# Kernel optimization log

Measured on AMD Instinct MI355X. Metric: run time of the kernel, lower is better.

## Reference

```python
import jax, jax.numpy as jnp
import numpy as np

B, S, F_IN, D, DFF, MEM, L, H = 32, 512, 64, 512, 2048, 1024, 3, 8
K_NEIGH = 3
TEMP = 1.0


def _pos_encoding(s, d):
    pos = np.arange(s, dtype=np.float64)[:, None]
    div = np.exp(np.arange(0, d, 2, dtype=np.float64) * (-np.log(10000.0) / d))
    pe = np.zeros((s, d), np.float32)
    pe[:, 0::2] = np.sin(pos * div)
    pe[:, 1::2] = np.cos(pos * div)
    return jnp.asarray(pe)


def _ln(x, g, b, eps=1e-5):
    m = x.mean(-1, keepdims=True)
    v = ((x - m) ** 2).mean(-1, keepdims=True)
    return (x - m) * jax.lax.rsqrt(v + eps) * g + b


def _mha(x, qkv_w, qkv_b, out_w, out_b):
    b, s, d = x.shape
    dh = d // H
    qkv = x @ qkv_w.T + qkv_b                      # (b,s,3d)
    q, k, v = jnp.split(qkv, 3, axis=-1)
    rs = lambda t: t.reshape(b, s, H, dh).transpose(0, 2, 1, 3)   # (b,h,s,dh)
    q, k, v = rs(q), rs(k), rs(v)
    scores = jnp.einsum('bhqd,bhkd->bhqk', q, k) / np.sqrt(dh).astype(np.float32)
    att = jax.nn.softmax(scores, axis=-1)
    o = jnp.einsum('bhqk,bhkd->bhqd', att, v).transpose(0, 2, 1, 3).reshape(b, s, d)
    return o @ out_w.T + out_b


def _construct_graph(x):
    # x: (B, S, F) -> adjacency (B, F, F) via kNN on rank-1 similarity (as in source)
    f = x.mean(axis=1)                                   # (B,F)
    n = jnp.linalg.norm(f, axis=1, keepdims=True)
    fn = f / jnp.maximum(n, 1e-12)                       # F.normalize over full vector
    sim = jnp.einsum('bi,bj->bij', fn, fn)               # (B,F,F)
    nf = f.shape[1]
    k = min(K_NEIGH, nf - 1)
    _, idx = jax.lax.top_k(sim, k + 1)                   # (B,F,k+1)
    idx = idx[..., 1:]                                   # drop top-1 (self under source's assumption)
    bidx = jnp.arange(f.shape[0])[:, None, None]
    ridx = jnp.arange(nf)[None, :, None]
    A = jnp.zeros((f.shape[0], nf, nf), x.dtype).at[bidx, ridx, idx].set(1.0)
    A = jnp.maximum(A, jnp.swapaxes(A, 1, 2))            # symmetrize
    di = jnp.arange(nf)
    return A.at[:, di, di].set(1.0)                      # fill_diagonal_(1)


def _gcn(x, A, w1, b1, w2, b2):
    deg = A.sum(2, keepdims=True)
    An = A / jnp.where(deg == 0, jnp.ones_like(deg), deg)
    xt = jnp.swapaxes(x, 1, 2)                           # (B,F,S)
    h = jax.nn.relu(jnp.einsum('bfg,bgh->bfh', An, xt @ w1.T + b1))
    h = jnp.einsum('bfg,bgh->bfh', An, h @ w2.T + b2)
    return jnp.swapaxes(h, 1, 2)                         # (B,S,F)


def _metg_forward(x, W_in, b_in, qkv_w, qkv_b, out_w, out_b, ln1_g, ln1_b,
                  ln2_g, ln2_b, ff1_w, ff1_b, ff2_w, ff2_b, memory,
                  fc1_w, fc1_b, fc2_w, fc2_b, gc1_w, gc1_b, gc2_w, gc2_b):
    # transformer branch
    h = x @ W_in.T + b_in                                # (B,S,D)
    h = h + _pos_encoding(h.shape[1], h.shape[2])
    for l in range(L):  # post-norm TransformerEncoderLayer, relu FFN, dropout=eval
        h = _ln(h + _mha(h, qkv_w[l], qkv_b[l], out_w[l], out_b[l]), ln1_g[l], ln1_b[l])
        ff = jax.nn.relu(h @ ff1_w[l].T + ff1_b[l]) @ ff2_w[l].T + ff2_b[l]
        h = _ln(h + ff, ln2_g[l], ln2_b[l])
    # memory module
    sims = (h @ memory.T) / TEMP                         # (B,S,MEM)
    attn = jax.nn.softmax(sims, axis=-1)
    upd = attn @ memory                                  # (B,S,D)
    # decoder
    cat = jnp.concatenate([h, upd], axis=-1)             # (B,S,2D)
    t_out = jax.nn.relu(cat @ fc1_w.T + fc1_b) @ fc2_w.T + fc2_b
    # GCN branch
    A = _construct_graph(x)
    g_out = _gcn(x, A, gc1_w, gc1_b, gc2_w, gc2_b)
    return t_out, g_out, attn


def setup_inputs() -> dict:
    key = jax.random.key(0)
    ks = jax.random.split(key, 12)
    w = lambda k, shape, s=0.02: jax.random.normal(k, shape, jnp.float32) * s
    return {
        'x': jax.random.normal(ks[0], (B, S, F_IN), jnp.float32),
        'W_in': w(ks[1], (D, F_IN)), 'b_in': jnp.zeros((D,), jnp.float32),
        'qkv_w': w(ks[2], (L, 3 * D, D)), 'qkv_b': jnp.zeros((L, 3 * D), jnp.float32),
        'out_w': w(ks[3], (L, D, D)), 'out_b': jnp.zeros((L, D), jnp.float32),
        'ln1_g': jnp.ones((L, D), jnp.float32), 'ln1_b': jnp.zeros((L, D), jnp.float32),
        'ln2_g': jnp.ones((L, D), jnp.float32), 'ln2_b': jnp.zeros((L, D), jnp.float32),
        'ff1_w': w(ks[4], (L, DFF, D)), 'ff1_b': jnp.zeros((L, DFF), jnp.float32),
        'ff2_w': w(ks[5], (L, D, DFF)), 'ff2_b': jnp.zeros((L, D), jnp.float32),
        'memory': w(ks[6], (MEM, D), 0.05),
        'fc1_w': w(ks[7], (D, 2 * D)), 'fc1_b': jnp.zeros((D,), jnp.float32),
        'fc2_w': w(ks[8], (F_IN, D)), 'fc2_b': jnp.zeros((F_IN,), jnp.float32),
        'gc1_w': w(ks[9], (D, S)), 'gc1_b': jnp.zeros((D,), jnp.float32),
        'gc2_w': w(ks[10], (S, D)), 'gc2_b': jnp.zeros((S,), jnp.float32),
    }


def reference(x, W_in, b_in, qkv_w, qkv_b, out_w, out_b, ln1_g, ln1_b,
              ln2_g, ln2_b, ff1_w, ff1_b, ff2_w, ff2_b, memory,
              fc1_w, fc1_b, fc2_w, fc2_b, gc1_w, gc1_b, gc2_w, gc2_b):
    return _metg_forward(x, W_in, b_in, qkv_w, qkv_b, out_w, out_b, ln1_g, ln1_b,
                         ln2_g, ln2_b, ff1_w, ff1_b, ff2_w, ff2_b, memory,
                         fc1_w, fc1_b, fc2_w, fc2_b, gc1_w, gc1_b, gc2_w, gc2_b)
```

## Files before the change

### kernel.cpp

```cpp
#include <hip/hip_runtime.h>
#include <hip/hip_bf16.h>
#include <math.h>


namespace {

typedef unsigned short ushort_t;
using bf16x8 = __attribute__((ext_vector_type(8))) __bf16;
using f32x4 = __attribute__((ext_vector_type(4))) float;
using ushort8 = __attribute__((ext_vector_type(8))) unsigned short;

constexpr int Mrows = 32 * 512;
constexpr size_t MB = 1048576;

__device__ __forceinline__ unsigned short f2bf(float f) {
  unsigned int u = __builtin_bit_cast(unsigned int, f);
  u += 0x7fffu + ((u >> 16) & 1u);
  return (unsigned short)(u >> 16);
}
__device__ __forceinline__ float bf2f(ushort_t u) {
  unsigned int v = ((unsigned int)u) << 16;
  return __builtin_bit_cast(float, v);
}

__device__ __forceinline__ void g2lds16(const void* g, void* l) {
  __builtin_amdgcn_global_load_lds(
      (const __attribute__((address_space(1))) unsigned int*)g,
      (__attribute__((address_space(3))) unsigned int*)l, 16, 0, 0);
}

template <bool RELU, bool BF16OUT>
__global__ __launch_bounds__(512, 2) void gemm256(const ushort_t* __restrict__ A,
                                                  const ushort_t* __restrict__ B,
                                                  const float* __restrict__ bias,
                                                  void* __restrict__ Cv,
                                                  int K, int lda, int ldc) {
  __shared__ __align__(16) ushort_t As[2][256 * 64];
  __shared__ __align__(16) ushort_t Bs[2][256 * 64];
  const int t = threadIdx.x;
  const int w = t >> 6, l = t & 63;
  const int m0 = blockIdx.x << 8, n0 = blockIdx.y << 8;
  const int srow8 = l >> 3;
  const int scol = ((l & 7) ^ srow8) << 3;
  const ushort_t* agp = A + (size_t)(m0 + w * 32 + srow8) * lda + scol;
  const ushort_t* bgp = B + (size_t)(n0 + w * 32 + srow8) * K + scol;
  const int wr = w >> 2, wcn = w & 3;
  const int lr = l & 15, g = l >> 4;
  const int sw = (l & 7) << 4;
  const int nt = K >> 6;
  f32x4 acc[8][4] = {};
#pragma unroll
  for (int i = 0; i < 4; ++i) {
    g2lds16(agp + (size_t)(i * 8) * lda, &As[0][(w * 32 + i * 8) * 64]);
    g2lds16(bgp + (size_t)(i * 8) * K, &Bs[0][(w * 32 + i * 8) * 64]);
  }
#pragma unroll
  for (int i = 0; i < 4; ++i) {
    g2lds16(agp + (size_t)(i * 8) * lda + 64, &As[1][(w * 32 + i * 8) * 64]);
    g2lds16(bgp + (size_t)(i * 8) * K + 64, &Bs[1][(w * 32 + i * 8) * 64]);
  }
  for (int j = 0; j < nt; ++j) {
    const int c = j & 1;
    asm volatile("s_waitcnt vmcnt(8)" ::: "memory");
    __builtin_amdgcn_s_barrier();
    asm volatile("" ::: "memory");
    const char* abase = (const char*)&As[c][0];
    const char* bbase = (const char*)&Bs[c][0];
#pragma unroll
    for (int ki = 0; ki < 2; ++ki) {
      const int kb = (ki * 64 + g * 16) ^ sw;
      bf16x8 af[8], bfr[4];
#pragma unroll
      for (int mi = 0; mi < 8; ++mi)
        af[mi] = *(const bf16x8*)(abase + (wr * 128 + mi * 16 + lr) * 128 + kb);
#pragma unroll
      for (int ni = 0; ni < 4; ++ni)
        bfr[ni] = *(const bf16x8*)(bbase + (wcn * 64 + ni * 16 + lr) * 128 + kb);
      __builtin_amdgcn_s_setprio(1);
#pragma unroll
      for (int mi = 0; mi < 8; ++mi)
#pragma unroll
        for (int ni = 0; ni < 4; ++ni)
          acc[mi][ni] = __builtin_amdgcn_mfma_f32_16x16x32_bf16(af[mi], bfr[ni],
                                                                acc[mi][ni], 0, 0, 0);
      __builtin_amdgcn_s_setprio(0);
    }
    asm volatile("s_waitcnt lgkmcnt(0)" ::: "memory");
    __builtin_amdgcn_s_barrier();
    asm volatile("" ::: "memory");
    if (j + 2 < nt) {
      const size_t ko = (size_t)(j + 2) * 64;
#pragma unroll
      for (int i = 0; i < 4; ++i) {
        g2lds16(agp + (size_t)(i * 8) * lda + ko, &As[c][(w * 32 + i * 8) * 64]);
        g2lds16(bgp + (size_t)(i * 8) * K + ko, &Bs[c][(w * 32 + i * 8) * 64]);
      }
    }
  }
  float bb[4];
#pragma unroll
  for (int ni = 0; ni < 4; ++ni) {
    const int ci = n0 + wcn * 64 + ni * 16 + lr;
    bb[ni] = bias ? bias[ci] : 0.f;
  }
  const int crow0 = m0 + wr * 128 + g * 4;
#pragma unroll
  for (int mi = 0; mi < 8; ++mi)
#pragma unroll
    for (int ni = 0; ni < 4; ++ni) {
      const int ci = n0 + wcn * 64 + ni * 16 + lr;
#pragma unroll
      for (int v = 0; v < 4; ++v) {
        float val = acc[mi][ni][v] + bb[ni];
        if (RELU) val = fmaxf(val, 0.f);
        const size_t off = (size_t)(crow0 + mi * 16 + v) * ldc + ci;
        if (BF16OUT) ((ushort_t*)Cv)[off] = f2bf(val);
        else         ((float*)Cv)[off] = val;
      }
    }
}

template <bool RELU, bool BF16OUT>
__global__ __launch_bounds__(256) void gemm_bf16(const ushort_t* __restrict__ A,
                                                 const ushort_t* __restrict__ B,
                                                 const float* __restrict__ bias,
                                                 void* __restrict__ Cv,
                                                 int K, int lda, int ldc, int Nclip) {
  __shared__ __align__(16) ushort_t As[128 * 64];
  __shared__ __align__(16) ushort_t Bs[128 * 64];
  const int t = threadIdx.x;
  const int w = t >> 6, l = t & 63;
  const int m0 = blockIdx.x << 7, n0 = blockIdx.y << 7;
  const int srow8 = l >> 3;
  const int scol = ((l & 7) ^ srow8) << 3;
  const ushort_t* agp = A + (size_t)(m0 + w * 32 + srow8) * lda + scol;
  const ushort_t* bgp = B + (size_t)(n0 + w * 32 + srow8) * K + scol;
  ushort_t* alds = &As[(w * 32) * 64];
  ushort_t* blds = &Bs[(w * 32) * 64];
  const int wr = w >> 1, wc = w & 1;
  const int lr = l & 15, g = l >> 4;
  const int sw = (l & 7) << 4;
  f32x4 acc[4][4] = {};
  for (int kt = 0; kt < K; kt += 64) {
    __syncthreads();
#pragma unroll
    for (int i = 0; i < 4; ++i) {
      g2lds16(agp + (size_t)(i * 8) * lda + kt, alds + i * 8 * 64);
      g2lds16(bgp + (size_t)(i * 8) * K + kt, blds + i * 8 * 64);
    }
    __syncthreads();
#pragma unroll
    for (int ki = 0; ki < 2; ++ki) {
      bf16x8 af[4], bf[4];
      const int kb = (ki * 64 + g * 16) ^ sw;
#pragma unroll
      for (int mi = 0; mi < 4; ++mi)
        af[mi] = *(const bf16x8*)((const char*)As + (wr * 64 + mi * 16 + lr) * 128 + kb);
#pragma unroll
      for (int ni = 0; ni < 4; ++ni)
        bf[ni] = *(const bf16x8*)((const char*)Bs + (wc * 64 + ni * 16 + lr) * 128 + kb);
#pragma unroll
      for (int mi = 0; mi < 4; ++mi)
#pragma unroll
        for (int ni = 0; ni < 4; ++ni)
          acc[mi][ni] = __builtin_amdgcn_mfma_f32_16x16x32_bf16(af[mi], bf[ni],
                                                                acc[mi][ni], 0, 0, 0);
    }
  }
  float bb[4];
#pragma unroll
  for (int ni = 0; ni < 4; ++ni) {
    const int ci = n0 + wc * 64 + ni * 16 + lr;
    bb[ni] = (bias && ci < Nclip) ? bias[ci] : 0.f;
  }
  const int crow0 = m0 + wr * 64 + g * 4;
#pragma unroll
  for (int mi = 0; mi < 4; ++mi)
#pragma unroll
    for (int ni = 0; ni < 4; ++ni) {
      const int ci = n0 + wc * 64 + ni * 16 + lr;
      if (ci >= Nclip) continue;
#pragma unroll
      for (int v = 0; v < 4; ++v) {
        float val = acc[mi][ni][v] + bb[ni];
        if (RELU) val = fmaxf(val, 0.f);
        const size_t off = (size_t)(crow0 + mi * 16 + v) * ldc + ci;
        if (BF16OUT) ((ushort_t*)Cv)[off] = f2bf(val);
        else         ((float*)Cv)[off] = val;
      }
    }
}

__global__ __launch_bounds__(256) void flash_attn_mfma(const ushort_t* __restrict__ qkvb,
                                                       ushort_t* __restrict__ ctxb) {
  __shared__ __align__(16) ushort_t Qs[64 * 64];
  __shared__ __align__(16) ushort_t Ks[64 * 64];
  __shared__ __align__(16) ushort_t VT[64 * 64];
  __shared__ __align__(16) ushort_t Ps[64 * 64];
  const int qb = blockIdx.x, hh = blockIdx.y, b = blockIdx.z;
  const int t = threadIdx.x, w = t >> 6, l = t & 63;
  const int g = l >> 4, lr = l & 15, l7 = l & 7;
  const ushort_t* qkv0 = qkvb + (size_t)b * 512 * 1536 + hh * 64;
  {
    const int r8 = l >> 3;
    const int gcol = (l7 ^ r8) << 3;
#pragma unroll
    for (int i = 0; i < 2; ++i) {
      const int row = w * 16 + i * 8 + r8;
      g2lds16(qkv0 + (size_t)(qb * 64 + row) * 1536 + gcol, &Qs[(w * 16 + i * 8) * 64]);
    }
  }
  float mst = -INFINITY, lst = 0.f;
  f32x4 oacc[4] = {};
  const int vk0 = (t & 31) * 2;
  const int vdh0 = (t >> 5) * 8;
  for (int kt = 0; kt < 8; ++kt) {
    __syncthreads();
    {
      const int r8 = l >> 3;
      const int gcol = (l7 ^ r8) << 3;
#pragma unroll
      for (int i = 0; i < 2; ++i) {
        const int row = w * 16 + i * 8 + r8;
        g2lds16(qkv0 + 512 + (size_t)(kt * 64 + row) * 1536 + gcol,
                &Ks[(w * 16 + i * 8) * 64]);
      }
    }
    {
      const ushort_t* vp = qkv0 + 1024 + (size_t)(kt * 64 + vk0) * 1536 + vdh0;
      ushort8 v0 = *(const ushort8*)vp;
      ushort8 v1 = *(const ushort8*)(vp + 1536);
      const int slotbase = vk0 >> 3;
      const int inb = (vk0 & 7) * 2;
#pragma unroll
      for (int e = 0; e < 8; ++e) {
        const int dh = vdh0 + e;
        unsigned int word = (unsigned int)v0[e] | ((unsigned int)v1[e] << 16);
        *(unsigned int*)((char*)VT + dh * 128 + (((slotbase ^ (dh & 7)) << 4) + inb)) = word;
      }
    }
    __syncthreads();
    f32x4 sacc[4] = {};
#pragma unroll
    for (int ki = 0; ki < 2; ++ki) {
      const int sb = ((ki * 4 + g) ^ l7) << 4;
      bf16x8 qf = *(const bf16x8*)((const char*)Qs + (w * 16 + lr) * 128 + sb);
#pragma unroll
      for (int mi = 0; mi < 4; ++mi) {
        bf16x8 kf = *(const bf16x8*)((const char*)Ks + (mi * 16 + lr) * 128 + sb);
        sacc[mi] = __builtin_amdgcn_mfma_f32_16x16x32_bf16(kf, qf, sacc[mi], 0, 0, 0);
      }
    }
    float p[4][4];
    float cmax = -INFINITY;
#pragma unroll
    for (int mi = 0; mi < 4; ++mi)
#pragma unroll
      for (int v = 0; v < 4; ++v) {
        p[mi][v] = sacc[mi][v] * 0.125f;
        cmax = fmaxf(cmax, p[mi][v]);
      }
    cmax = fmaxf(cmax, __shfl_xor(cmax, 16));
    cmax = fmaxf(cmax, __shfl_xor(cmax, 32));
    const float mnew = fmaxf(mst, cmax);
    const float al = __expf(mst - mnew);
    float csum = 0.f;
#pragma unroll
    for (int mi = 0; mi < 4; ++mi)
#pragma unroll
      for (int v = 0; v < 4; ++v) {
        p[mi][v] = __expf(p[mi][v] - mnew);
        csum += p[mi][v];
      }
    csum += __shfl_xor(csum, 16);
    csum += __shfl_xor(csum, 32);
    lst = lst * al + csum;
    mst = mnew;
#pragma unroll
    for (int mi = 0; mi < 4; ++mi) oacc[mi] *= al;
    {
      char* pbase = (char*)Ps + (w * 16 + lr) * 128;
#pragma unroll
      for (int mi = 0; mi < 4; ++mi)
#pragma unroll
        for (int vp2 = 0; vp2 < 2; ++vp2) {
          const int klo = mi * 16 + g * 4 + vp2 * 2;
          unsigned int word = (unsigned int)f2bf(p[mi][vp2 * 2]) |
                              ((unsigned int)f2bf(p[mi][vp2 * 2 + 1]) << 16);
          *(unsigned int*)(pbase + (((klo >> 3) ^ l7) << 4) + (klo & 7) * 2) = word;
        }
    }
#pragma unroll
    for (int ki = 0; ki < 2; ++ki) {
      const int sb = ((ki * 4 + g) ^ l7) << 4;
      bf16x8 pf = *(const bf16x8*)((const char*)Ps + (w * 16 + lr) * 128 + sb);
#pragma unroll
      for (int mi = 0; mi < 4; ++mi) {
        bf16x8 vf = *(const bf16x8*)((const char*)VT + (mi * 16 + lr) * 128 + sb);
        oacc[mi] = __builtin_amdgcn_mfma_f32_16x16x32_bf16(vf, pf, oacc[mi], 0, 0, 0);
      }
    }
  }
  const float inv = 1.f / lst;
  ushort_t* op = ctxb + (size_t)(b * 512 + qb * 64 + w * 16 + lr) * 512 + hh * 64;
#pragma unroll
  for (int mi = 0; mi < 4; ++mi)
#pragma unroll
    for (int vp2 = 0; vp2 < 2; ++vp2) {
      const int dh = mi * 16 + g * 4 + vp2 * 2;
      unsigned int word = (unsigned int)f2bf(oacc[mi][vp2 * 2] * inv) |
                          ((unsigned int)f2bf(oacc[mi][vp2 * 2 + 1] * inv) << 16);
      *(unsigned int*)(op + dh) = word;
    }
}

#define OUTER16(ACC, A4, B4) do { \
  ACC[0][0] += (A4).x*(B4).x; ACC[0][1] += (A4).x*(B4).y; ACC[0][2] += (A4).x*(B4).z; ACC[0][3] += (A4).x*(B4).w; \
  ACC[1][0] += (A4).y*(B4).x; ACC[1][1] += (A4).y*(B4).y; ACC[1][2] += (A4).y*(B4).z; ACC[1][3] += (A4).y*(B4).w; \
  ACC[2][0] += (A4).z*(B4).x; ACC[2][1] += (A4).z*(B4).y; ACC[2][2] += (A4).z*(B4).z; ACC[2][3] += (A4).z*(B4).w; \
  ACC[3][0] += (A4).w*(B4).x; ACC[3][1] += (A4).w*(B4).y; ACC[3][2] += (A4).w*(B4).z; ACC[3][3] += (A4).w*(B4).w; \
} while (0)

__global__ __launch_bounds__(256) void win_pe_gemm(const float* __restrict__ A,
                                                   const float* __restrict__ Bm,
                                                   const float* __restrict__ bias,
                                                   const float* __restrict__ peb,
                                                   ushort_t* __restrict__ hbb) {
  __shared__ float As[16][68];
  __shared__ float Bs[16][68];
  const int t = threadIdx.x;
  const int m0 = blockIdx.x << 6;
  const int n0 = blockIdx.y << 6;
  const int r0 = (t >> 4) << 2;
  const int c0 = (t & 15) << 2;
  const int lm = t >> 2;
  const int lk4 = (t & 3) << 2;
  float acc[4][4] = {{0.f, 0.f, 0.f, 0.f}, {0.f, 0.f, 0.f, 0.f},
                     {0.f, 0.f, 0.f, 0.f}, {0.f, 0.f, 0.f, 0.f}};
  for (int kt = 0; kt < 64; kt += 16) {
    __syncthreads();
    float4 av = *reinterpret_cast<const float4*>(A + (size_t)(m0 + lm) * 64 + kt + lk4);
    As[lk4 + 0][lm] = av.x; As[lk4 + 1][lm] = av.y;
    As[lk4 + 2][lm] = av.z; As[lk4 + 3][lm] = av.w;
    float4 bv = *reinterpret_cast<const float4*>(Bm + (size_t)(n0 + lm) * 64 + kt + lk4);
    Bs[lk4 + 0][lm] = bv.x; Bs[lk4 + 1][lm] = bv.y;
    Bs[lk4 + 2][lm] = bv.z; Bs[lk4 + 3][lm] = bv.w;
    __syncthreads();
#pragma unroll
    for (int k = 0; k < 16; ++k) {
      float4 a4 = *reinterpret_cast<const float4*>(&As[k][r0]);
      float4 b4 = *reinterpret_cast<const float4*>(&Bs[k][c0]);
      OUTER16(acc, a4, b4);
    }
  }
  const float bb0 = bias[n0 + c0 + 0], bb1 = bias[n0 + c0 + 1];
  const float bb2 = bias[n0 + c0 + 2], bb3 = bias[n0 + c0 + 3];
#pragma unroll
  for (int i = 0; i < 4; ++i) {
    const int row = m0 + r0 + i;
    float4 p = *reinterpret_cast<const float4*>(peb + (size_t)(row & 511) * 512 + n0 + c0);
    ushort4 ob;
    ob.x = f2bf(acc[i][0] + bb0 + p.x);
    ob.y = f2bf(acc[i][1] + bb1 + p.y);
    ob.z = f2bf(acc[i][2] + bb2 + p.z);
    ob.w = f2bf(acc[i][3] + bb3 + p.w);
    *reinterpret_cast<ushort4*>(hbb + (size_t)row * 512 + n0 + c0) = ob;
  }
}

__global__ __launch_bounds__(256) void ln_wave(const ushort_t* __restrict__ hbi,
                                               const ushort_t* __restrict__ resb,
                                               const float* __restrict__ g,
                                               const float* __restrict__ bt,
                                               ushort_t* __restrict__ hbo, int hbs) {
  const int t = threadIdx.x;
  const size_t row = (size_t)blockIdx.x * 4 + (t >> 6);
  const int lane = t & 63;
  const size_t base = row * 512 + lane * 8;
  ushort8 hv = *reinterpret_cast<const ushort8*>(hbi + base);
  ushort8 rv = *reinterpret_cast<const ushort8*>(resb + base);
  float xs[8];
  float sum = 0.f;
#pragma unroll
  for (int i = 0; i < 8; ++i) { xs[i] = bf2f(hv[i]) + bf2f(rv[i]); sum += xs[i]; }
#pragma unroll
  for (int off = 1; off < 64; off <<= 1) sum += __shfl_xor(sum, off);
  const float mean = sum * (1.f / 512.f);
  float vs = 0.f;
#pragma unroll
  for (int i = 0; i < 8; ++i) { xs[i] -= mean; vs += xs[i] * xs[i]; }
#pragma unroll
  for (int off = 1; off < 64; off <<= 1) vs += __shfl_xor(vs, off);
  const float rstd = rsqrtf(vs * (1.f / 512.f) + 1e-5f);
  float4 g0 = *reinterpret_cast<const float4*>(g + lane * 8);
  float4 g1 = *reinterpret_cast<const float4*>(g + lane * 8 + 4);
  float4 b0 = *reinterpret_cast<const float4*>(bt + lane * 8);
  float4 b1 = *reinterpret_cast<const float4*>(bt + lane * 8 + 4);
  ushort8 o;
  o[0] = f2bf(xs[0] * rstd * g0.x + b0.x); o[1] = f2bf(xs[1] * rstd * g0.y + b0.y);
  o[2] = f2bf(xs[2] * rstd * g0.z + b0.z); o[3] = f2bf(xs[3] * rstd * g0.w + b0.w);
  o[4] = f2bf(xs[4] * rstd * g1.x + b1.x); o[5] = f2bf(xs[5] * rstd * g1.y + b1.y);
  o[6] = f2bf(xs[6] * rstd * g1.z + b1.z); o[7] = f2bf(xs[7] * rstd * g1.w + b1.w);
  *reinterpret_cast<ushort8*>(hbo + row * hbs + lane * 8) = o;
}

__global__ __launch_bounds__(256) void softmax_wave(const ushort_t* __restrict__ simsb,
                                                    float* __restrict__ attn,
                                                    ushort_t* __restrict__ attnb) {
  const int t = threadIdx.x;
  const size_t row = (size_t)blockIdx.x * 4 + (t >> 6);
  const int lane = t & 63;
  const size_t base = row * 1024 + lane * 16;
  ushort8 v0 = *reinterpret_cast<const ushort8*>(simsb + base);
  ushort8 v1 = *reinterpret_cast<const ushort8*>(simsb + base + 8);
  float xs[16];
  float mx = -INFINITY;
#pragma unroll
  for (int i = 0; i < 8; ++i) { xs[i] = bf2f(v0[i]); xs[i + 8] = bf2f(v1[i]); }
#pragma unroll
  for (int i = 0; i < 16; ++i) mx = fmaxf(mx, xs[i]);
#pragma unroll
  for (int off = 1; off < 64; off <<= 1) mx = fmaxf(mx, __shfl_xor(mx, off));
  float sum = 0.f;
#pragma unroll
  for (int i = 0; i < 16; ++i) { xs[i] = __expf(xs[i] - mx); sum += xs[i]; }
#pragma unroll
  for (int off = 1; off < 64; off <<= 1) sum += __shfl_xor(sum, off);
  const float inv = 1.f / sum;
  ushort8 o0, o1;
#pragma unroll
  for (int i = 0; i < 16; ++i) xs[i] *= inv;
#pragma unroll
  for (int i = 0; i < 4; ++i) {
    float4 f = make_float4(xs[4 * i], xs[4 * i + 1], xs[4 * i + 2], xs[4 * i + 3]);
    *reinterpret_cast<float4*>(attn + base + 4 * i) = f;
  }
#pragma unroll
  for (int i = 0; i < 8; ++i) { o0[i] = f2bf(xs[i]); o1[i] = f2bf(xs[i + 8]); }
  *reinterpret_cast<ushort8*>(attnb + base) = o0;
  *reinterpret_cast<ushort8*>(attnb + base + 8) = o1;
}

__global__ void pe_kernel(float* __restrict__ pe) {
  const int s = blockIdx.x, i = threadIdx.x;
  double div = exp((double)(2 * i) * (-log(10000.0) / 512.0));
  double a = (double)s * div;
  pe[s * 512 + 2 * i] = (float)sin(a);
  pe[s * 512 + 2 * i + 1] = (float)cos(a);
}

__global__ __launch_bounds__(256) void cvt_all(
    const float* __restrict__ qkvw, const float* __restrict__ outw,
    const float* __restrict__ ff1w, const float* __restrict__ ff2w,
    const float* __restrict__ memw, const float* __restrict__ fc1w,
    const float* __restrict__ gc1w, const float* __restrict__ gc2w,
    const float* __restrict__ fc2w,
    ushort_t* qkvb, ushort_t* outb, ushort_t* ff1b, ushort_t* ff2b,
    ushort_t* memb, ushort_t* fc1b, ushort_t* gc1b, ushort_t* gc2b,
    ushort_t* fc2p) {
  const int gidx = blockIdx.x * 256 + threadIdx.x;
  if (gidx >= 2768896) return;
  if (gidx >= 2752512) {
    const int off = gidx - 2752512;
    ushort4 o = {0, 0, 0, 0};
    if (off < 8192) {
      float4 v = reinterpret_cast<const float4*>(fc2w)[off];
      o.x = f2bf(v.x); o.y = f2bf(v.y); o.z = f2bf(v.z); o.w = f2bf(v.w);
    }
    reinterpret_cast<ushort4*>(fc2p)[off] = o;
    return;
  }
  const float* s; ushort_t* d; int off;
  if (gidx < 589824)        { s = qkvw; d = qkvb; off = gidx; }
  else if (gidx < 786432)   { s = outw; d = outb; off = gidx - 589824; }
  else if (gidx < 1572864)  { s = ff1w; d = ff1b; off = gidx - 786432; }
  else if (gidx < 2359296)  { s = ff2w; d = ff2b; off = gidx - 1572864; }
  else if (gidx < 2490368)  { s = memw; d = memb; off = gidx - 2359296; }
  else if (gidx < 2621440)  { s = fc1w; d = fc1b; off = gidx - 2490368; }
  else if (gidx < 2686976)  { s = gc1w; d = gc1b; off = gidx - 2621440; }
  else                      { s = gc2w; d = gc2b; off = gidx - 2686976; }
  float4 v = reinterpret_cast<const float4*>(s)[off];
  ushort4 o;
  o.x = f2bf(v.x); o.y = f2bf(v.y); o.z = f2bf(v.z); o.w = f2bf(v.w);
  reinterpret_cast<ushort4*>(d)[off] = o;
}

__global__ __launch_bounds__(256) void transpose_cvt(const float* __restrict__ in,
                                                     ushort_t* __restrict__ out) {
  const int g = blockIdx.x * 256 + threadIdx.x;
  const int r = g >> 9, c = g & 511;
  out[(size_t)c * 1024 + r] = f2bf(in[g]);
}

__global__ __launch_bounds__(256) void transpose_x_bf16(const float* __restrict__ x,
                                                        ushort_t* __restrict__ xtb) {
  __shared__ float Ls[64][65];
  const int sc = blockIdx.x, b = blockIdx.y;
  const int t = threadIdx.x;
  const int f = t & 63, sr = t >> 6;
#pragma unroll
  for (int j = 0; j < 16; ++j) {
    const int s = sr + 4 * j;
    Ls[s][f] = x[((size_t)(b * 512 + sc * 64 + s)) * 64 + f];
  }
  __syncthreads();
#pragma unroll
  for (int j = 0; j < 16; ++j) {
    const int fr = sr * 16 + j;
    xtb[((size_t)b * 64 + fr) * 512 + sc * 64 + f] = f2bf(Ls[f][fr]);
  }
}

__global__ __launch_bounds__(256) void fmean2(const float* __restrict__ x,
                                              float* __restrict__ fn) {
  __shared__ float part[4][64];
  const int b = blockIdx.x, t = threadIdx.x;
  const int f = t & 63, sg = t >> 6;
  float acc = 0.f;
  const float* xp = x + ((size_t)b * 512 + sg) * 64 + f;
  for (int s = sg; s < 512; s += 4, xp += 256) acc += *xp;
  part[sg][f] = acc;
  __syncthreads();
  if (t < 64) {
    float m = (part[0][t] + part[1][t] + part[2][t] + part[3][t]) * (1.f / 512.f);
    float ss = m * m;
#pragma unroll
    for (int off = 32; off; off >>= 1) ss += __shfl_xor(ss, off);
    float n = fmaxf(sqrtf(ss), 1e-12f);
    fn[b * 64 + t] = m / n;
  }
}

__global__ __launch_bounds__(256) void graph_kernel2(const float* __restrict__ fn,
                                                     float* __restrict__ An) {
  __shared__ float fv[64];
  __shared__ float Am[64][65];
  const int b = blockIdx.x, t = threadIdx.x;
  const int i = t >> 2, g = t & 3;
  if (t < 64) fv[t] = fn[b * 64 + t];
#pragma unroll
  for (int j = 0; j < 16; ++j) Am[i][g * 16 + j] = 0.f;
  __syncthreads();
  const float fi = fv[i];
  unsigned int mask = 0;
  int sel[4];
  for (int r = 0; r < 4; ++r) {
    float best = -INFINITY;
    int bi = 1 << 30;
    for (int j = 0; j < 16; ++j) {
      if (mask & (1u << j)) continue;
      float v = fi * fv[g * 16 + j];
      if (v > best) { best = v; bi = g * 16 + j; }
    }
#pragma unroll
    for (int off = 1; off < 4; off <<= 1) {
      float ov = __shfl_xor(best, off);
      int oi = __shfl_xor(bi, off);
      if (ov > best || (ov == best && oi < bi)) { best = ov; bi = oi; }
    }
    sel[r] = bi;
    if ((bi >> 4) == g) mask |= 1u << (bi & 15);
  }
  if (g == 0) { Am[i][sel[1]] = 1.f; Am[i][sel[2]] = 1.f; Am[i][sel[3]] = 1.f; }
  __syncthreads();
  float vals[16];
  float deg = 0.f;
#pragma unroll
  for (int j0 = 0; j0 < 16; ++j0) {
    const int j = g * 16 + j0;
    float v = (j == i) ? 1.f : fmaxf(Am[i][j], Am[j][i]);
    vals[j0] = v;
    deg += v;
  }
#pragma unroll
  for (int off = 1; off < 4; off <<= 1) deg += __shfl_xor(deg, off);
  const float inv = 1.f / deg;
  float* out = An + ((size_t)b * 64 + i) * 64 + g * 16;
#pragma unroll
  for (int j0 = 0; j0 < 16; ++j0) out[j0] = vals[j0] * inv;
}

template <bool RELU, bool STORE_T>
__global__ __launch_bounds__(256) void bmm_an(const float* __restrict__ An,
                                              const float* __restrict__ X,
                                              float* __restrict__ Y,
                                              ushort_t* __restrict__ Yb) {
  __shared__ float Ag[64][68];
  __shared__ float Xs[64][68];
  const int nc = blockIdx.x << 6;
  const int b = blockIdx.y;
  const int t = threadIdx.x;
  {
    const int i = t >> 2, g0 = (t & 3) << 4;
    const float* ap = An + ((size_t)b * 64 + i) * 64 + g0;
#pragma unroll
    for (int j = 0; j < 16; ++j) Ag[g0 + j][i] = ap[j];
  }
  {
    const int g = t >> 2, n4 = (t & 3) << 4;
    const float* xp = X + ((size_t)b * 64 + g) * 512 + nc + n4;
#pragma unroll
    for (int j = 0; j < 4; ++j)
      *reinterpret_cast<float4*>(&Xs[g][n4 + 4 * j]) =
          *reinterpret_cast<const float4*>(xp + 4 * j);
  }
  __syncthreads();
  const int r0 = (t >> 4) << 2, c0 = (t & 15) << 2;
  float acc[4][4] = {{0.f, 0.f, 0.f, 0.f}, {0.f, 0.f, 0.f, 0.f},
                     {0.f, 0.f, 0.f, 0.f}, {0.f, 0.f, 0.f, 0.f}};
#pragma unroll 8
  for (int g = 0; g < 64; ++g) {
    float4 a4 = *reinterpret_cast<const float4*>(&Ag[g][r0]);
    float4 x4 = *reinterpret_cast<const float4*>(&Xs[g][c0]);
    OUTER16(acc, a4, x4);
  }
  if (!STORE_T) {
#pragma unroll
    for (int i = 0; i < 4; ++i) {
      float4 o = make_float4(acc[i][0], acc[i][1], acc[i][2], acc[i][3]);
      if (RELU) {
        o.x = fmaxf(o.x, 0.f); o.y = fmaxf(o.y, 0.f);
        o.z = fmaxf(o.z, 0.f); o.w = fmaxf(o.w, 0.f);
      }
      ushort4 ob;
      ob.x = f2bf(o.x); ob.y = f2bf(o.y); ob.z = f2bf(o.z); ob.w = f2bf(o.w);
      *reinterpret_cast<ushort4*>(Yb + ((size_t)b * 64 + r0 + i) * 512 + nc + c0) = ob;
    }
  } else {
#pragma unroll
    for (int j = 0; j < 4; ++j) {
      float4 o = make_float4(acc[0][j], acc[1][j], acc[2][j], acc[3][j]);
      *reinterpret_cast<float4*>(Y + ((size_t)b * 512 + nc + c0 + j) * 64 + r0) = o;
    }
  }
}

}

extern "C" void kernel_launch(void* const* d_in, const int* in_sizes, int n_in,
                              void* d_out, int out_size, void* d_ws, size_t ws_size,
                              hipStream_t stream) {
  const float* x     = (const float*)d_in[0];
  const float* W_in  = (const float*)d_in[1];
  const float* b_in  = (const float*)d_in[2];
  const float* qkv_w = (const float*)d_in[3];
  const float* qkv_b = (const float*)d_in[4];
  const float* out_w = (const float*)d_in[5];
  const float* out_b = (const float*)d_in[6];
  const float* ln1_g = (const float*)d_in[7];
  const float* ln1_b = (const float*)d_in[8];
  const float* ln2_g = (const float*)d_in[9];
  const float* ln2_b = (const float*)d_in[10];
  const float* ff1_w = (const float*)d_in[11];
  const float* ff1_b = (const float*)d_in[12];
  const float* ff2_w = (const float*)d_in[13];
  const float* ff2_b = (const float*)d_in[14];
  const float* memw  = (const float*)d_in[15];
  const float* fc1_w = (const float*)d_in[16];
  const float* fc1_b = (const float*)d_in[17];
  const float* fc2_w = (const float*)d_in[18];
  const float* fc2_b = (const float*)d_in[19];
  const float* gc1_w = (const float*)d_in[20];
  const float* gc1_b = (const float*)d_in[21];
  const float* gc2_w = (const float*)d_in[22];
  const float* gc2_b = (const float*)d_in[23];

  char* wsb = (char*)d_ws;
  ushort_t* hb     = (ushort_t*)(wsb + 0);
  ushort_t* ctxb   = (ushort_t*)(wsb + 16 * MB);
  ushort_t* resb   = (ushort_t*)(wsb + 32 * MB);
  char*     U1     = wsb + 48 * MB;
  float*    pe     = (float*)(wsb + 144 * MB);
  ushort_t* qkv_wb = (ushort_t*)(wsb + 146 * MB);
  ushort_t* out_wb = (ushort_t*)(wsb + 151 * MB);
  ushort_t* ff1_wb = (ushort_t*)(wsb + 153 * MB);
  ushort_t* ff2_wb = (ushort_t*)(wsb + 160 * MB);
  ushort_t* mem_b  = (ushort_t*)(wsb + 166 * MB);
  ushort_t* memT_b = (ushort_t*)(wsb + 167 * MB);
  ushort_t* fc1_wb = (ushort_t*)(wsb + 168 * MB);
  ushort_t* gc1_wb = (ushort_t*)(wsb + 169 * MB);
  ushort_t* gc2_wb = (ushort_t*)(wsb + 169 * MB + 524288);
  ushort_t* fc2_wp = (ushort_t*)(wsb + 170 * MB);
  float*    fn     = (float*)(wsb + 171 * MB);
  float*    An     = (float*)(wsb + 172 * MB);

  ushort_t* qkvb    = (ushort_t*)U1;
  ushort_t* midb    = (ushort_t*)U1;
  ushort_t* catb    = (ushort_t*)U1;
  ushort_t* simsb   = (ushort_t*)(U1 + 32 * MB);
  ushort_t* attnb   = (ushort_t*)(U1 + 64 * MB);
  ushort_t* fc1outb = (ushort_t*)(U1 + 64 * MB);
  ushort_t* xtb  = (ushort_t*)U1;
  float*    t1   = (float*)(U1 + 2 * MB);
  ushort_t* h1b  = (ushort_t*)(U1 + 6 * MB);
  float*    t2   = (float*)(U1 + 8 * MB);

  float* t_out = (float*)d_out;
  float* g_out = t_out + 1048576;
  float* attn  = g_out + 1048576;

  hipLaunchKernelGGL(cvt_all, dim3(10816), dim3(256), 0, stream,
                     qkv_w, out_w, ff1_w, ff2_w, memw, fc1_w, gc1_w, gc2_w, fc2_w,
                     qkv_wb, out_wb, ff1_wb, ff2_wb, mem_b, fc1_wb, gc1_wb, gc2_wb,
                     fc2_wp);
  hipLaunchKernelGGL(transpose_cvt, dim3(2048), dim3(256), 0, stream, memw, memT_b);
  hipLaunchKernelGGL(pe_kernel, dim3(512), dim3(256), 0, stream, pe);

  hipLaunchKernelGGL(win_pe_gemm, dim3(256, 8), dim3(256), 0, stream,
                     x, W_in, b_in, pe, hb);

  for (int l = 0; l < 3; ++l) {
    hipLaunchKernelGGL((gemm256<false, true>), dim3(64, 6), dim3(512), 0, stream,
                       hb, qkv_wb + (size_t)l * 786432, qkv_b + l * 1536, qkvb,
                       512, 512, 1536);
    hipLaunchKernelGGL(flash_attn_mfma, dim3(8, 8, 32), dim3(256), 0, stream, qkvb, ctxb);
    hipLaunchKernelGGL((gemm_bf16<false, true>), dim3(128, 4), dim3(256), 0, stream,
                       ctxb, out_wb + (size_t)l * 262144, out_b + l * 512, resb,
                       512, 512, 512, 512);
    hipLaunchKernelGGL(ln_wave, dim3(Mrows / 4), dim3(256), 0, stream,
                       hb, resb, ln1_g + l * 512, ln1_b + l * 512, hb, 512);
    hipLaunchKernelGGL((gemm256<true, true>), dim3(64, 8), dim3(512), 0, stream,
                       hb, ff1_wb + (size_t)l * 1048576, ff1_b + l * 2048, midb,
                       512, 512, 2048);
    hipLaunchKernelGGL((gemm_bf16<false, true>), dim3(128, 4), dim3(256), 0, stream,
                       midb, ff2_wb + (size_t)l * 1048576, ff2_b + l * 512, resb,
                       2048, 2048, 512, 512);
    if (l < 2) {
      hipLaunchKernelGGL(ln_wave, dim3(Mrows / 4), dim3(256), 0, stream,
                         hb, resb, ln2_g + l * 512, ln2_b + l * 512, hb, 512);
    } else {
      hipLaunchKernelGGL(ln_wave, dim3(Mrows / 4), dim3(256), 0, stream,
                         hb, resb, ln2_g + l * 512, ln2_b + l * 512, catb, 1024);
    }
  }

  hipLaunchKernelGGL((gemm256<false, true>), dim3(64, 4), dim3(512), 0, stream,
                     catb, mem_b, (const float*)nullptr, simsb,
                     512, 1024, 1024);
  hipLaunchKernelGGL(softmax_wave, dim3(Mrows / 4), dim3(256), 0, stream,
                     simsb, attn, attnb);
  hipLaunchKernelGGL((gemm_bf16<false, true>), dim3(128, 4), dim3(256), 0, stream,
                     attnb, memT_b, (const float*)nullptr, catb + 512,
                     1024, 1024, 1024, 512);
  hipLaunchKernelGGL((gemm_bf16<true, true>), dim3(128, 4), dim3(256), 0, stream,
                     catb, fc1_wb, fc1_b, fc1outb, 1024, 1024, 512, 512);
  hipLaunchKernelGGL((gemm_bf16<false, false>), dim3(128, 1), dim3(256), 0, stream,
                     fc1outb, fc2_wp, fc2_b, t_out, 512, 512, 64, 64);

  hipLaunchKernelGGL(fmean2, dim3(32), dim3(256), 0, stream, x, fn);
  hipLaunchKernelGGL(graph_kernel2, dim3(32), dim3(256), 0, stream, fn, An);
  hipLaunchKernelGGL(transpose_x_bf16, dim3(8, 32), dim3(256), 0, stream, x, xtb);
  hipLaunchKernelGGL((gemm_bf16<false, false>), dim3(16, 4), dim3(256), 0, stream,
                     xtb, gc1_wb, gc1_b, t1, 512, 512, 512, 512);
  hipLaunchKernelGGL((bmm_an<true, false>), dim3(8, 32), dim3(256), 0, stream,
                     An, t1, (float*)nullptr, h1b);
  hipLaunchKernelGGL((gemm_bf16<false, false>), dim3(16, 4), dim3(256), 0, stream,
                     h1b, gc2_wb, gc2_b, t2, 512, 512, 512, 512);
  hipLaunchKernelGGL((bmm_an<false, true>), dim3(8, 32), dim3(256), 0, stream,
                     An, t2, g_out, (ushort_t*)nullptr);
}
```

Baseline: 900.9 us.

## Interleave half-tile LDS prefetch with quarter-tile MFMA phases in gemm256

The gemm256 main loop is rebuilt as an unrolled two-stage schedule. Each 64-wide K tile is split into four MFMA phases over half M and half N fragments, and the global-to-LDS loads for the next tiles are issued in 128-row halves between those phases, with barriers and explicit vmcnt waits around them. The goal is to overlap memory traffic with matrix math more evenly and lower register pressure from fragment loads. The cost is many more s_barrier calls per tile, and the loop now assumes the number of K tiles is even. The flash-attention grid also swaps the head and query-block axes, so that blocks sharing a query block run next to each other for better cache locality.

```diff
diff --git a/kernel.cpp b/kernel.cpp
--- a/kernel.cpp
+++ b/kernel.cpp
@@ -40,63 +40,101 @@
   const int t = threadIdx.x;
   const int w = t >> 6, l = t & 63;
   const int m0 = blockIdx.x << 8, n0 = blockIdx.y << 8;
-  const int srow8 = l >> 3;
-  const int scol = ((l & 7) ^ srow8) << 3;
-  const ushort_t* agp = A + (size_t)(m0 + w * 32 + srow8) * lda + scol;
-  const ushort_t* bgp = B + (size_t)(n0 + w * 32 + srow8) * K + scol;
+  const int r8 = l >> 3;
+  const int scol = ((l & 7) ^ r8) << 3;
+  const size_t aoff = (size_t)(m0 + w * 16 + r8) * lda + scol;
+  const size_t boff = (size_t)(n0 + w * 16 + r8) * K + scol;
   const int wr = w >> 2, wcn = w & 3;
   const int lr = l & 15, g = l >> 4;
   const int sw = (l & 7) << 4;
+  const int kb0 = (g * 16) ^ sw;
+  const int kb1 = (64 + g * 16) ^ sw;
+  const char* Ab0 = (const char*)&As[0][0];
+  const char* Ab1 = (const char*)&As[1][0];
+  const char* Bb0 = (const char*)&Bs[0][0];
+  const char* Bb1 = (const char*)&Bs[1][0];
   const int nt = K >> 6;
   f32x4 acc[8][4] = {};
-#pragma unroll
-  for (int i = 0; i < 4; ++i) {
-    g2lds16(agp + (size_t)(i * 8) * lda, &As[0][(w * 32 + i * 8) * 64]);
-    g2lds16(bgp + (size_t)(i * 8) * K, &Bs[0][(w * 32 + i * 8) * 64]);
-  }
-#pragma unroll
-  for (int i = 0; i < 4; ++i) {
-    g2lds16(agp + (size_t)(i * 8) * lda + 64, &As[1][(w * 32 + i * 8) * 64]);
-    g2lds16(bgp + (size_t)(i * 8) * K + 64, &Bs[1][(w * 32 + i * 8) * 64]);
-  }
-  for (int j = 0; j < nt; ++j) {
-    const int c = j & 1;
-    asm volatile("s_waitcnt vmcnt(8)" ::: "memory");
-    __builtin_amdgcn_s_barrier();
-    asm volatile("" ::: "memory");
-    const char* abase = (const char*)&As[c][0];
-    const char* bbase = (const char*)&Bs[c][0];
-#pragma unroll
-    for (int ki = 0; ki < 2; ++ki) {
-      const int kb = (ki * 64 + g * 16) ^ sw;
-      bf16x8 af[8], bfr[4];
-#pragma unroll
-      for (int mi = 0; mi < 8; ++mi)
-        af[mi] = *(const bf16x8*)(abase + (wr * 128 + mi * 16 + lr) * 128 + kb);
-#pragma unroll
-      for (int ni = 0; ni < 4; ++ni)
-        bfr[ni] = *(const bf16x8*)(bbase + (wcn * 64 + ni * 16 + lr) * 128 + kb);
-      __builtin_amdgcn_s_setprio(1);
-#pragma unroll
-      for (int mi = 0; mi < 8; ++mi)
-#pragma unroll
-        for (int ni = 0; ni < 4; ++ni)
-          acc[mi][ni] = __builtin_amdgcn_mfma_f32_16x16x32_bf16(af[mi], bfr[ni],
-                                                                acc[mi][ni], 0, 0, 0);
-      __builtin_amdgcn_s_setprio(0);
-    }
-    asm volatile("s_waitcnt lgkmcnt(0)" ::: "memory");
-    __builtin_amdgcn_s_barrier();
-    asm volatile("" ::: "memory");
-    if (j + 2 < nt) {
-      const size_t ko = (size_t)(j + 2) * 64;
-#pragma unroll
-      for (int i = 0; i < 4; ++i) {
-        g2lds16(agp + (size_t)(i * 8) * lda + ko, &As[c][(w * 32 + i * 8) * 64]);
-        g2lds16(bgp + (size_t)(i * 8) * K + ko, &Bs[c][(w * 32 + i * 8) * 64]);
-      }
-    }
-  }
+  bf16x8 af[4][2];
+  bf16x8 bf[4][2];
+
+#define ST_A(d, h, tk) do { \
+    const ushort_t* _s = A + aoff + (size_t)(h) * 128 * lda + (size_t)(tk) * 64; \
+    g2lds16(_s, &As[d][((h) * 128 + w * 16) * 64]); \
+    g2lds16(_s + (size_t)8 * lda, &As[d][((h) * 128 + w * 16 + 8) * 64]); \
+  } while (0)
+#define ST_B(d, h, tk) do { \
+    const ushort_t* _s = B + boff + (size_t)(h) * 128 * K + (size_t)(tk) * 64; \
+    g2lds16(_s, &Bs[d][((h) * 128 + w * 16) * 64]); \
+    g2lds16(_s + (size_t)8 * K, &Bs[d][((h) * 128 + w * 16 + 8) * 64]); \
+  } while (0)
+#define RD_A(AB, MIH) do { \
+    _Pragma("unroll") for (int m = 0; m < 4; ++m) { \
+      af[m][0] = *(const bf16x8*)(AB + (wr * 128 + ((MIH) * 4 + m) * 16 + lr) * 128 + kb0); \
+      af[m][1] = *(const bf16x8*)(AB + (wr * 128 + ((MIH) * 4 + m) * 16 + lr) * 128 + kb1); } \
+  } while (0)
+#define RD_B(BB, NIH) do { \
+    _Pragma("unroll") for (int n = 0; n < 2; ++n) { \
+      bf[(NIH) * 2 + n][0] = *(const bf16x8*)(BB + (wcn * 64 + ((NIH) * 2 + n) * 16 + lr) * 128 + kb0); \
+      bf[(NIH) * 2 + n][1] = *(const bf16x8*)(BB + (wcn * 64 + ((NIH) * 2 + n) * 16 + lr) * 128 + kb1); } \
+  } while (0)
+#define MMA(MIH, NIH) do { \
+    __builtin_amdgcn_s_setprio(1); \
+    _Pragma("unroll") for (int ki = 0; ki < 2; ++ki) \
+      _Pragma("unroll") for (int m = 0; m < 4; ++m) \
+        _Pragma("unroll") for (int n = 0; n < 2; ++n) \
+          acc[(MIH) * 4 + m][(NIH) * 2 + n] = __builtin_amdgcn_mfma_f32_16x16x32_bf16( \
+              af[m][ki], bf[(NIH) * 2 + n][ki], acc[(MIH) * 4 + m][(NIH) * 2 + n], 0, 0, 0); \
+    __builtin_amdgcn_s_setprio(0); \
+  } while (0)
+#define BAR() __builtin_amdgcn_s_barrier()
+
+  ST_A(0, 0, 0); ST_A(0, 1, 0); ST_B(0, 0, 0); ST_B(0, 1, 0);
+  ST_B(1, 0, 1); ST_A(1, 0, 1);
+  asm volatile("s_waitcnt vmcnt(4)" ::: "memory");
+  __builtin_amdgcn_sched_barrier(0);
+  BAR();
+
+  for (int j = 0; j < (nt >> 1); ++j) {
+    const int t1 = 2 * j + 1, t2 = 2 * j + 2, t3 = 2 * j + 3;
+    RD_A(Ab0, 0); RD_B(Bb0, 0);
+    ST_B(1, 1, t1);
+    BAR(); MMA(0, 0); BAR();
+    RD_B(Bb0, 1);
+    ST_A(1, 1, t1);
+    BAR(); MMA(0, 1); BAR();
+    RD_A(Ab0, 1);
+    if (t2 < nt) ST_B(0, 0, t2);
+    BAR(); MMA(1, 0);
+    BAR();
+    if (t2 < nt) ST_A(0, 0, t2);
+    BAR(); MMA(1, 1);
+    asm volatile("s_waitcnt vmcnt(4)" ::: "memory");
+    __builtin_amdgcn_sched_barrier(0);
+    BAR();
+    RD_A(Ab1, 0); RD_B(Bb1, 0);
+    if (t2 < nt) ST_B(0, 1, t2);
+    BAR(); MMA(0, 0); BAR();
+    RD_B(Bb1, 1);
+    if (t2 < nt) ST_A(0, 1, t2);
+    BAR(); MMA(0, 1); BAR();
+    RD_A(Ab1, 1);
+    if (t3 < nt) ST_B(1, 0, t3);
+    BAR(); MMA(1, 0);
+    BAR();
+    if (t3 < nt) ST_A(1, 0, t3);
+    BAR(); MMA(1, 1);
+    asm volatile("s_waitcnt vmcnt(4)" ::: "memory");
+    __builtin_amdgcn_sched_barrier(0);
+    BAR();
+  }
+#undef ST_A
+#undef ST_B
+#undef RD_A
+#undef RD_B
+#undef MMA
+#undef BAR
+
   float bb[4];
 #pragma unroll
   for (int ni = 0; ni < 4; ++ni) {
@@ -197,7 +235,7 @@
   __shared__ __align__(16) ushort_t Ks[64 * 64];
   __shared__ __align__(16) ushort_t VT[64 * 64];
   __shared__ __align__(16) ushort_t Ps[64 * 64];
-  const int qb = blockIdx.x, hh = blockIdx.y, b = blockIdx.z;
+  const int hh = blockIdx.x, qb = blockIdx.y, b = blockIdx.z;
   const int t = threadIdx.x, w = t >> 6, l = t & 63;
   const int g = l >> 4, lr = l & 15, l7 = l & 7;
   const ushort_t* qkv0 = qkvb + (size_t)b * 512 * 1536 + hh * 64;
```

Result: no change. 894.1 us (-0.8%).

## Process two query tiles per flash-attention block and fuse graph mean kernels

Applied to the files above, without the earlier changes.

Each flash-attention block now handles 128 query rows as two 64-row halves, so every K and V tile loaded into shared memory is reused twice. This halves K/V global traffic and the V transpose work, and the grid shrinks to half as many blocks, reordered so heads vary fastest. Separately, the feature-mean kernel and the graph kNN kernel are merged into one launch, which removes a launch and the intermediate normalized-feature buffer. The cost is more shared memory and registers per block and fewer blocks in flight.

```diff
diff --git a/kernel.cpp b/kernel.cpp
--- a/kernel.cpp
+++ b/kernel.cpp
@@ -193,11 +193,11 @@
 
 __global__ __launch_bounds__(256) void flash_attn_mfma(const ushort_t* __restrict__ qkvb,
                                                        ushort_t* __restrict__ ctxb) {
-  __shared__ __align__(16) ushort_t Qs[64 * 64];
+  __shared__ __align__(16) ushort_t Qs[2][64 * 64];
   __shared__ __align__(16) ushort_t Ks[64 * 64];
   __shared__ __align__(16) ushort_t VT[64 * 64];
-  __shared__ __align__(16) ushort_t Ps[64 * 64];
-  const int qb = blockIdx.x, hh = blockIdx.y, b = blockIdx.z;
+  __shared__ __align__(16) ushort_t Ps[2][64 * 64];
+  const int hh = blockIdx.x, qb = blockIdx.y, b = blockIdx.z;
   const int t = threadIdx.x, w = t >> 6, l = t & 63;
   const int g = l >> 4, lr = l & 15, l7 = l & 7;
   const ushort_t* qkv0 = qkvb + (size_t)b * 512 * 1536 + hh * 64;
@@ -205,13 +205,16 @@
     const int r8 = l >> 3;
     const int gcol = (l7 ^ r8) << 3;
 #pragma unroll
-    for (int i = 0; i < 2; ++i) {
-      const int row = w * 16 + i * 8 + r8;
-      g2lds16(qkv0 + (size_t)(qb * 64 + row) * 1536 + gcol, &Qs[(w * 16 + i * 8) * 64]);
-    }
-  }
-  float mst = -INFINITY, lst = 0.f;
-  f32x4 oacc[4] = {};
+    for (int qh = 0; qh < 2; ++qh)
+#pragma unroll
+      for (int i = 0; i < 2; ++i) {
+        const int row = qb * 128 + qh * 64 + w * 16 + i * 8 + r8;
+        g2lds16(qkv0 + (size_t)row * 1536 + gcol, &Qs[qh][(w * 16 + i * 8) * 64]);
+      }
+  }
+  float mst[2] = {-INFINITY, -INFINITY};
+  float lst[2] = {0.f, 0.f};
+  f32x4 oacc[2][4] = {};
   const int vk0 = (t & 31) * 2;
   const int vdh0 = (t >> 5) * 8;
   for (int kt = 0; kt < 8; ++kt) {
@@ -240,78 +243,86 @@
       }
     }
     __syncthreads();
-    f32x4 sacc[4] = {};
-#pragma unroll
-    for (int ki = 0; ki < 2; ++ki) {
-      const int sb = ((ki * 4 + g) ^ l7) << 4;
-      bf16x8 qf = *(const bf16x8*)((const char*)Qs + (w * 16 + lr) * 128 + sb);
-#pragma unroll
-      for (int mi = 0; mi < 4; ++mi) {
-        bf16x8 kf = *(const bf16x8*)((const char*)Ks + (mi * 16 + lr) * 128 + sb);
-        sacc[mi] = __builtin_amdgcn_mfma_f32_16x16x32_bf16(kf, qf, sacc[mi], 0, 0, 0);
-      }
-    }
-    float p[4][4];
-    float cmax = -INFINITY;
+#pragma unroll
+    for (int qh = 0; qh < 2; ++qh) {
+      f32x4 sacc[4] = {};
+#pragma unroll
+      for (int ki = 0; ki < 2; ++ki) {
+        const int sb = ((ki * 4 + g) ^ l7) << 4;
+        bf16x8 qf = *(const bf16x8*)((const char*)&Qs[qh][0] + (w * 16 + lr) * 128 + sb);
+#pragma unroll
+        for (int mi = 0; mi < 4; ++mi) {
+          bf16x8 kf = *(const bf16x8*)((const char*)Ks + (mi * 16 + lr) * 128 + sb);
+          sacc[mi] = __builtin_amdgcn_mfma_f32_16x16x32_bf16(kf, qf, sacc[mi], 0, 0, 0);
+        }
+      }
+      float p[4][4];
+      float cmax = -INFINITY;
+#pragma unroll
+      for (int mi = 0; mi < 4; ++mi)
+#pragma unroll
+        for (int v = 0; v < 4; ++v) {
+          p[mi][v] = sacc[mi][v] * 0.125f;
+          cmax = fmaxf(cmax, p[mi][v]);
+        }
+      cmax = fmaxf(cmax, __shfl_xor(cmax, 16));
+      cmax = fmaxf(cmax, __shfl_xor(cmax, 32));
+      const float mnew = fmaxf(mst[qh], cmax);
+      const float al = __expf(mst[qh] - mnew);
+      float csum = 0.f;
+#pragma unroll
+      for (int mi = 0; mi < 4; ++mi)
+#pragma unroll
+        for (int v = 0; v < 4; ++v) {
+          p[mi][v] = __expf(p[mi][v] - mnew);
+          csum += p[mi][v];
+        }
+      csum += __shfl_xor(csum, 16);
+      csum += __shfl_xor(csum, 32);
+      lst[qh] = lst[qh] * al + csum;
+      mst[qh] = mnew;
+#pragma unroll
+      for (int mi = 0; mi < 4; ++mi) oacc[qh][mi] *= al;
+      {
+        char* pbase = (char*)&Ps[qh][0] + (w * 16 + lr) * 128;
+#pragma unroll
+        for (int mi = 0; mi < 4; ++mi)
+#pragma unroll
+          for (int vp2 = 0; vp2 < 2; ++vp2) {
+            const int klo = mi * 16 + g * 4 + vp2 * 2;
+            unsigned int word = (unsigned int)f2bf(p[mi][vp2 * 2]) |
+                                ((unsigned int)f2bf(p[mi][vp2 * 2 + 1]) << 16);
+            *(unsigned int*)(pbase + (((klo >> 3) ^ l7) << 4) + (klo & 7) * 2) = word;
+          }
+      }
+#pragma unroll
+      for (int ki = 0; ki < 2; ++ki) {
+        const int sb = ((ki * 4 + g) ^ l7) << 4;
+        bf16x8 pf = *(const bf16x8*)((const char*)&Ps[qh][0] + (w * 16 + lr) * 128 + sb);
+#pragma unroll
+        for (int mi = 0; mi < 4; ++mi) {
+          bf16x8 vf = *(const bf16x8*)((const char*)VT + (mi * 16 + lr) * 128 + sb);
+          oacc[qh][mi] = __builtin_amdgcn_mfma_f32_16x16x32_bf16(vf, pf, oacc[qh][mi],
+                                                                 0, 0, 0);
+        }
+      }
+    }
+  }
+#pragma unroll
+  for (int qh = 0; qh < 2; ++qh) {
+    const float inv = 1.f / lst[qh];
+    ushort_t* op = ctxb +
+        (size_t)(b * 512 + qb * 128 + qh * 64 + w * 16 + lr) * 512 + hh * 64;
 #pragma unroll
     for (int mi = 0; mi < 4; ++mi)
 #pragma unroll
-      for (int v = 0; v < 4; ++v) {
-        p[mi][v] = sacc[mi][v] * 0.125f;
-        cmax = fmaxf(cmax, p[mi][v]);
-      }
-    cmax = fmaxf(cmax, __shfl_xor(cmax, 16));
-    cmax = fmaxf(cmax, __shfl_xor(cmax, 32));
-    const float mnew = fmaxf(mst, cmax);
-    const float al = __expf(mst - mnew);
-    float csum = 0.f;
-#pragma unroll
-    for (int mi = 0; mi < 4; ++mi)
-#pragma unroll
-      for (int v = 0; v < 4; ++v) {
-        p[mi][v] = __expf(p[mi][v] - mnew);
-        csum += p[mi][v];
-      }
-    csum += __shfl_xor(csum, 16);
-    csum += __shfl_xor(csum, 32);
-    lst = lst * al + csum;
-    mst = mnew;
-#pragma unroll
-    for (int mi = 0; mi < 4; ++mi) oacc[mi] *= al;
-    {
-      char* pbase = (char*)Ps + (w * 16 + lr) * 128;
-#pragma unroll
-      for (int mi = 0; mi < 4; ++mi)
-#pragma unroll
-        for (int vp2 = 0; vp2 < 2; ++vp2) {
-          const int klo = mi * 16 + g * 4 + vp2 * 2;
-          unsigned int word = (unsigned int)f2bf(p[mi][vp2 * 2]) |
-                              ((unsigned int)f2bf(p[mi][vp2 * 2 + 1]) << 16);
-          *(unsigned int*)(pbase + (((klo >> 3) ^ l7) << 4) + (klo & 7) * 2) = word;
-        }
-    }
-#pragma unroll
-    for (int ki = 0; ki < 2; ++ki) {
-      const int sb = ((ki * 4 + g) ^ l7) << 4;
-      bf16x8 pf = *(const bf16x8*)((const char*)Ps + (w * 16 + lr) * 128 + sb);
-#pragma unroll
-      for (int mi = 0; mi < 4; ++mi) {
-        bf16x8 vf = *(const bf16x8*)((const char*)VT + (mi * 16 + lr) * 128 + sb);
-        oacc[mi] = __builtin_amdgcn_mfma_f32_16x16x32_bf16(vf, pf, oacc[mi], 0, 0, 0);
-      }
-    }
-  }
-  const float inv = 1.f / lst;
-  ushort_t* op = ctxb + (size_t)(b * 512 + qb * 64 + w * 16 + lr) * 512 + hh * 64;
-#pragma unroll
-  for (int mi = 0; mi < 4; ++mi)
-#pragma unroll
-    for (int vp2 = 0; vp2 < 2; ++vp2) {
-      const int dh = mi * 16 + g * 4 + vp2 * 2;
-      unsigned int word = (unsigned int)f2bf(oacc[mi][vp2 * 2] * inv) |
-                          ((unsigned int)f2bf(oacc[mi][vp2 * 2 + 1] * inv) << 16);
-      *(unsigned int*)(op + dh) = word;
-    }
+      for (int vp2 = 0; vp2 < 2; ++vp2) {
+        const int dh = mi * 16 + g * 4 + vp2 * 2;
+        unsigned int word = (unsigned int)f2bf(oacc[qh][mi][vp2 * 2] * inv) |
+                            ((unsigned int)f2bf(oacc[qh][mi][vp2 * 2 + 1] * inv) << 16);
+        *(unsigned int*)(op + dh) = word;
+      }
+  }
 }
 
 #define OUTER16(ACC, A4, B4) do { \
@@ -511,15 +522,20 @@
   }
 }
 
-__global__ __launch_bounds__(256) void fmean2(const float* __restrict__ x,
-                                              float* __restrict__ fn) {
+__global__ __launch_bounds__(256) void fmean_graph(const float* __restrict__ x,
+                                                   float* __restrict__ An) {
   __shared__ float part[4][64];
+  __shared__ float fv[64];
+  __shared__ float Am[64][65];
   const int b = blockIdx.x, t = threadIdx.x;
   const int f = t & 63, sg = t >> 6;
+  const int i = t >> 2, g = t & 3;
   float acc = 0.f;
   const float* xp = x + ((size_t)b * 512 + sg) * 64 + f;
   for (int s = sg; s < 512; s += 4, xp += 256) acc += *xp;
   part[sg][f] = acc;
+#pragma unroll
+  for (int j = 0; j < 16; ++j) Am[i][g * 16 + j] = 0.f;
   __syncthreads();
   if (t < 64) {
     float m = (part[0][t] + part[1][t] + part[2][t] + part[3][t]) * (1.f / 512.f);
@@ -527,19 +543,8 @@
 #pragma unroll
     for (int off = 32; off; off >>= 1) ss += __shfl_xor(ss, off);
     float n = fmaxf(sqrtf(ss), 1e-12f);
-    fn[b * 64 + t] = m / n;
-  }
-}
-
-__global__ __launch_bounds__(256) void graph_kernel2(const float* __restrict__ fn,
-                                                     float* __restrict__ An) {
-  __shared__ float fv[64];
-  __shared__ float Am[64][65];
-  const int b = blockIdx.x, t = threadIdx.x;
-  const int i = t >> 2, g = t & 3;
-  if (t < 64) fv[t] = fn[b * 64 + t];
-#pragma unroll
-  for (int j = 0; j < 16; ++j) Am[i][g * 16 + j] = 0.f;
+    fv[t] = m / n;
+  }
   __syncthreads();
   const float fi = fv[i];
   unsigned int mask = 0;
@@ -681,7 +686,6 @@
   ushort_t* gc1_wb = (ushort_t*)(wsb + 169 * MB);
   ushort_t* gc2_wb = (ushort_t*)(wsb + 169 * MB + 524288);
   ushort_t* fc2_wp = (ushort_t*)(wsb + 170 * MB);
-  float*    fn     = (float*)(wsb + 171 * MB);
   float*    An     = (float*)(wsb + 172 * MB);
 
   ushort_t* qkvb    = (ushort_t*)U1;
@@ -713,7 +717,7 @@
     hipLaunchKernelGGL((gemm256<false, true>), dim3(64, 6), dim3(512), 0, stream,
                        hb, qkv_wb + (size_t)l * 786432, qkv_b + l * 1536, qkvb,
                        512, 512, 1536);
-    hipLaunchKernelGGL(flash_attn_mfma, dim3(8, 8, 32), dim3(256), 0, stream, qkvb, ctxb);
+    hipLaunchKernelGGL(flash_attn_mfma, dim3(8, 4, 32), dim3(256), 0, stream, qkvb, ctxb);
     hipLaunchKernelGGL((gemm_bf16<false, true>), dim3(128, 4), dim3(256), 0, stream,
                        ctxb, out_wb + (size_t)l * 262144, out_b + l * 512, resb,
                        512, 512, 512, 512);
@@ -747,8 +751,7 @@
   hipLaunchKernelGGL((gemm_bf16<false, false>), dim3(128, 1), dim3(256), 0, stream,
                      fc1outb, fc2_wp, fc2_b, t_out, 512, 512, 64, 64);
 
-  hipLaunchKernelGGL(fmean2, dim3(32), dim3(256), 0, stream, x, fn);
-  hipLaunchKernelGGL(graph_kernel2, dim3(32), dim3(256), 0, stream, fn, An);
+  hipLaunchKernelGGL(fmean_graph, dim3(32), dim3(256), 0, stream, x, An);
   hipLaunchKernelGGL(transpose_x_bf16, dim3(8, 32), dim3(256), 0, stream, x, xtb);
   hipLaunchKernelGGL((gemm_bf16<false, false>), dim3(16, 4), dim3(256), 0, stream,
                      xtb, gc1_wb, gc1_b, t1, 512, 512, 512, 512);
```

After: 911.4 us. Within noise of the previous version (+1.2%).
